# Kernel optimization log

Measured on AMD Instinct MI355X. Metric: run time of the kernel, lower is better.

Reference implementation:

```python
import jax, jax.numpy as jnp
import numpy as np

N_HEAD = 16
HEAD_DIM = 64  # n_embd // n_head = 1024 // 16


def setup_inputs() -> dict:
    key = jax.random.key(0)
    k1, k2, k3 = jax.random.split(key, 3)
    B, S, D = 2, 2048, 1024
    x = jax.random.normal(k1, (B, S, D), dtype=jnp.float32)
    # torch nn.Linear stores weight [out, in]; we keep [in, out] for x @ W
    w_qkv = jax.random.normal(k2, (D, 3 * D), dtype=jnp.float32) * (D ** -0.5)
    w_proj = jax.random.normal(k3, (D, D), dtype=jnp.float32) * (D ** -0.5)
    return {"x": x, "w_qkv": w_qkv, "w_proj": w_proj}


def reference(x, w_qkv, w_proj):
    B, S, D = x.shape
    qkv = x @ w_qkv  # [B, S, 3D]
    q, k, v = jnp.split(qkv, 3, axis=-1)
    # [B, H, S, hd]
    q = q.reshape(B, S, N_HEAD, HEAD_DIM).transpose(0, 2, 1, 3)
    k = k.reshape(B, S, N_HEAD, HEAD_DIM).transpose(0, 2, 1, 3)
    v = v.reshape(B, S, N_HEAD, HEAD_DIM).transpose(0, 2, 1, 3)
    att = jnp.einsum('bhid,bhjd->bhij', q, k) * (HEAD_DIM ** -0.5)
    causal = jnp.tril(jnp.ones((S, S), dtype=bool))
    att = jnp.where(causal, att, jnp.finfo(att.dtype).min)
    att = jax.nn.softmax(att, axis=-1)
    # dropout p=0 (eval) -> identity
    y = jnp.einsum('bhij,bhjd->bhid', att, v)
    y = y.transpose(0, 2, 1, 3).reshape(B, S, D)
    return y @ w_proj
```

## Files before the change

kernel.cpp:

```cpp
#include <hip/hip_runtime.h>

#define AS1 __attribute__((address_space(1)))
#define AS3 __attribute__((address_space(3)))

using f32x4 = __attribute__((ext_vector_type(4))) float;
using s16x8 = __attribute__((ext_vector_type(8))) short;
using u16x4 = __attribute__((ext_vector_type(4))) unsigned short;
using u32x2 = __attribute__((ext_vector_type(2))) unsigned int;

__device__ __forceinline__ unsigned short f2bf(float f) {
  union { float f; unsigned u; } v; v.f = f;
  unsigned u = v.u;
  return (unsigned short)((u + 0x7FFFu + ((u >> 16) & 1u)) >> 16);
}

__device__ __forceinline__ unsigned pack_bf2(float a, float b) {
  union { float f; unsigned u; } x, y; x.f = a; y.f = b;
  return (x.u >> 16) | (y.u & 0xFFFF0000u);
}

__device__ __forceinline__ void load_lds16(const void* g, void* l) {
  __builtin_amdgcn_global_load_lds((const AS1 void*)g, (AS3 void*)l, 16, 0, 0);
}

__global__ __launch_bounds__(256) void prep_kernel(const float* __restrict__ x,
                                                   const float* __restrict__ w_qkv,
                                                   const float* __restrict__ w_proj,
                                                   unsigned short* __restrict__ xb,
                                                   unsigned short* __restrict__ wqkvT,
                                                   unsigned short* __restrict__ wprojT) {
  __shared__ float tile[32][33];
  const int bid = blockIdx.x, tid = threadIdx.x;
  if (bid < 4096) {
    int i = bid * 256 + tid;
    float4 v = ((const float4*)x)[i];
    u16x4 o;
    o.x = f2bf(v.x); o.y = f2bf(v.y); o.z = f2bf(v.z); o.w = f2bf(v.w);
    ((u16x4*)xb)[i] = o;
    return;
  }
  const float* in;
  unsigned short* out;
  int bx, by, R, C;
  if (bid < 7168) {
    int t = bid - 4096;
    bx = t % 96; by = t / 96; R = 1024; C = 3072;
    in = w_qkv; out = wqkvT;
  } else {
    int t = bid - 7168;
    bx = t % 32; by = t / 32; R = 1024; C = 1024;
    in = w_proj; out = wprojT;
  }
  const int tx = tid & 31, ty = tid >> 5;
  int xcol = bx * 32 + tx;
  int y0 = by * 32;
  for (int j = ty; j < 32; j += 8)
    tile[j][tx] = in[(size_t)(y0 + j) * C + xcol];
  __syncthreads();
  int x2 = by * 32 + tx;
  int y2 = bx * 32;
  for (int j = ty; j < 32; j += 8)
    out[(size_t)(y2 + j) * R + x2] = f2bf(tile[tx][j]);
}

__global__ __launch_bounds__(256) void transpose_v(const unsigned short* __restrict__ qkv,
                                                   unsigned short* __restrict__ Vt) {
  __shared__ unsigned short tile[64][65];
  const int tid = threadIdx.x;
  const int bh = blockIdx.y, b = bh >> 4, h = bh & 15;
  const int s0 = blockIdx.x * 64;
#pragma unroll
  for (int it = 0; it < 2; ++it) {
    int c = tid + it * 256;
    int row = c >> 3, cc = c & 7;
    s16x8 v = *(const s16x8*)(qkv + (size_t)(b * 2048 + s0 + row) * 3072 + 2048 + h * 64 + cc * 8);
#pragma unroll
    for (int j = 0; j < 8; ++j) tile[row][cc * 8 + j] = (unsigned short)v[j];
  }
  __syncthreads();
#pragma unroll
  for (int it = 0; it < 2; ++it) {
    int c = tid + it * 256;
    int d = c >> 3, sc = c & 7;
    s16x8 o;
#pragma unroll
    for (int j = 0; j < 8; ++j) o[j] = (short)tile[sc * 8 + j][d];
    *(s16x8*)(Vt + (size_t)bh * 64 * 2048 + (size_t)d * 2048 + s0 + sc * 8) = o;
  }
}

__global__ __launch_bounds__(256) void gemm_qkv(const unsigned short* __restrict__ A,
                                                const unsigned short* __restrict__ Bt,
                                                unsigned short* __restrict__ C,
                                                int M, int N, int K) {
  __shared__ unsigned short As[128 * 64];
  __shared__ unsigned short Bs[128 * 64];
  const int tid = threadIdx.x;
  const int wave = tid >> 6, lane = tid & 63;
  const int l15 = lane & 15, quad = lane >> 4;
  const int sx = l15 & 7;
  const int wm = wave & 1, wn = wave >> 1;
  const int bm = blockIdx.y, bn = blockIdx.x;

  f32x4 acc[4][4] = {};

  for (int k0 = 0; k0 < K; k0 += 64) {
    __syncthreads();
#pragma unroll
    for (int s = 0; s < 4; ++s) {
      int c = tid + s * 256;
      int row = c >> 3, cc = c & 7;
      int kc = (cc ^ (row & 7)) * 8;
      load_lds16(A + (size_t)(bm * 128 + row) * K + k0 + kc, As + c * 8);
      load_lds16(Bt + (size_t)(bn * 128 + row) * K + k0 + kc, Bs + c * 8);
    }
    __syncthreads();
#pragma unroll
    for (int kk = 0; kk < 2; ++kk) {
      s16x8 af[4], bfr[4];
#pragma unroll
      for (int i = 0; i < 4; ++i) {
        af[i]  = *(const s16x8*)(As + (wm * 64 + i * 16 + l15) * 64 + ((quad + 4 * kk) ^ sx) * 8);
        bfr[i] = *(const s16x8*)(Bs + (wn * 64 + i * 16 + l15) * 64 + ((quad + 4 * kk) ^ sx) * 8);
      }
#pragma unroll
      for (int i = 0; i < 4; ++i)
#pragma unroll
        for (int j = 0; j < 4; ++j)
          acc[i][j] = __builtin_amdgcn_mfma_f32_16x16x32_bf16(af[i], bfr[j], acc[i][j], 0, 0, 0);
    }
  }

  const int row0 = bm * 128 + wm * 64 + quad * 4;
  const int col0 = bn * 128 + wn * 64 + l15;
#pragma unroll
  for (int i = 0; i < 4; ++i)
#pragma unroll
    for (int j = 0; j < 4; ++j)
#pragma unroll
      for (int r = 0; r < 4; ++r)
        C[(size_t)(row0 + i * 16 + r) * N + (col0 + j * 16)] = f2bf(acc[i][j][r]);
}

__global__ __launch_bounds__(256) void gemm_proj(const unsigned short* __restrict__ A,
                                                 const unsigned short* __restrict__ Bt,
                                                 float* __restrict__ C,
                                                 int M, int N, int K) {
  __shared__ unsigned short As[128 * 64];
  __shared__ unsigned short Bs[64 * 64];
  const int tid = threadIdx.x;
  const int wave = tid >> 6, lane = tid & 63;
  const int l15 = lane & 15, quad = lane >> 4;
  const int sx = l15 & 7;
  const int wm = wave & 1, wn = wave >> 1;
  const int bm = blockIdx.y, bn = blockIdx.x;

  f32x4 acc[4][2] = {};

  for (int k0 = 0; k0 < K; k0 += 64) {
    __syncthreads();
#pragma unroll
    for (int s = 0; s < 4; ++s) {
      int c = tid + s * 256;
      int row = c >> 3, cc = c & 7;
      int kc = (cc ^ (row & 7)) * 8;
      load_lds16(A + (size_t)(bm * 128 + row) * K + k0 + kc, As + c * 8);
    }
#pragma unroll
    for (int s = 0; s < 2; ++s) {
      int c = tid + s * 256;
      int row = c >> 3, cc = c & 7;
      int kc = (cc ^ (row & 7)) * 8;
      load_lds16(Bt + (size_t)(bn * 64 + row) * K + k0 + kc, Bs + c * 8);
    }
    __syncthreads();
#pragma unroll
    for (int kk = 0; kk < 2; ++kk) {
      s16x8 af[4], bfr[2];
#pragma unroll
      for (int i = 0; i < 4; ++i)
        af[i] = *(const s16x8*)(As + (wm * 64 + i * 16 + l15) * 64 + ((quad + 4 * kk) ^ sx) * 8);
#pragma unroll
      for (int j = 0; j < 2; ++j)
        bfr[j] = *(const s16x8*)(Bs + (wn * 32 + j * 16 + l15) * 64 + ((quad + 4 * kk) ^ sx) * 8);
#pragma unroll
      for (int i = 0; i < 4; ++i)
#pragma unroll
        for (int j = 0; j < 2; ++j)
          acc[i][j] = __builtin_amdgcn_mfma_f32_16x16x32_bf16(af[i], bfr[j], acc[i][j], 0, 0, 0);
    }
  }

  const int row0 = bm * 128 + wm * 64 + quad * 4;
  const int col0 = bn * 64 + wn * 32 + l15;
#pragma unroll
  for (int i = 0; i < 4; ++i)
#pragma unroll
    for (int j = 0; j < 2; ++j)
#pragma unroll
      for (int r = 0; r < 4; ++r)
        C[(size_t)(row0 + i * 16 + r) * N + (col0 + j * 16)] = acc[i][j][r];
}

__global__ __launch_bounds__(512) void attn_kernel(const unsigned short* __restrict__ qkv,
                                                   const unsigned short* __restrict__ Vt,
                                                   unsigned short* __restrict__ Y) {
  __shared__ unsigned short Qs[128 * 64];
  __shared__ unsigned short Ks[2][64 * 64];
  __shared__ unsigned short Vs[2][64 * 64];
  const int tid = threadIdx.x;
  const int wave = tid >> 6, lane = tid & 63;
  const int l15 = lane & 15, quad = lane >> 4;
  const int sx = l15 & 7, sx2 = sx << 1;

  const int p = blockIdx.x;
  const int r_ = p >> 8, c_ = p & 255;
  const int m_ = c_ & 15, g_ = c_ >> 4;
  const int bh = g_ + 16 * r_;
  const int lq = r_ ? (15 - m_) : m_;
  const int q0 = lq * 128;
  const int b = bh >> 4, h = bh & 15;
  const size_t base = (size_t)b * 2048 * 3072 + h * 64;
  const size_t vbase = (size_t)bh * 64 * 2048;

  const int srow = tid >> 3, scc = tid & 7;
  const int skc = (scc ^ (srow & 7)) * 8;

#pragma unroll
  for (int s = 0; s < 2; ++s) {
    int cid = tid + s * 512;
    int row = cid >> 3, cc = cid & 7;
    int kc = (cc ^ (row & 7)) * 8;
    load_lds16(qkv + base + (size_t)(q0 + row) * 3072 + kc, Qs + cid * 8);
  }
  load_lds16(qkv + base + (size_t)srow * 3072 + 1024 + skc, Ks[0] + tid * 8);
  load_lds16(Vt + vbase + (size_t)srow * 2048 + skc, Vs[0] + tid * 8);
  __syncthreads();

  s16x8 qf[2];
  qf[0] = *(const s16x8*)(Qs + (wave * 16 + l15) * 64 + ((quad    ) ^ sx) * 8);
  qf[1] = *(const s16x8*)(Qs + (wave * 16 + l15) * 64 + ((quad + 4) ^ sx) * 8);

  f32x4 o[4] = {};
  float m_i = -1e30f, l_i = 0.f;
  const float kScale = 0.125f * 1.44269504f;
  const int qrow_w0 = q0 + wave * 16;
  const int qrow = qrow_w0 + l15;
  unsigned short* Pw = Qs + wave * 16 * 64;

  const int jmax = q0 + 64;
  int cur = 0;

  for (int j0 = 0; j0 <= jmax; j0 += 64) {
    if (j0 < jmax) {
      load_lds16(qkv + base + (size_t)(j0 + 64 + srow) * 3072 + 1024 + skc, Ks[cur ^ 1] + tid * 8);
      load_lds16(Vt + vbase + (size_t)srow * 2048 + (j0 + 64) + skc, Vs[cur ^ 1] + tid * 8);
    }

    if (j0 <= qrow_w0 + 15) {
      const unsigned short* Kc = Ks[cur];
      const unsigned short* Vc = Vs[cur];
      f32x4 s[4];
#pragma unroll
      for (int nt = 0; nt < 4; ++nt) {
        const int kr = nt * 16 + l15;
        s16x8 kf0 = *(const s16x8*)(Kc + kr * 64 + ((quad    ) ^ sx) * 8);
        s16x8 kf1 = *(const s16x8*)(Kc + kr * 64 + ((quad + 4) ^ sx) * 8);
        f32x4 z = {};
        z = __builtin_amdgcn_mfma_f32_16x16x32_bf16(kf0, qf[0], z, 0, 0, 0);
        z = __builtin_amdgcn_mfma_f32_16x16x32_bf16(kf1, qf[1], z, 0, 0, 0);
        s[nt] = z;
      }

      if (j0 + 63 > qrow_w0) {
#pragma unroll
        for (int nt = 0; nt < 4; ++nt) {
          int key0 = j0 + nt * 16 + quad * 4;
#pragma unroll
          for (int r = 0; r < 4; ++r)
            if (key0 + r > qrow) s[nt][r] = -3e38f;
        }
      }

      float t0 = fmaxf(fmaxf(s[0][0], s[0][1]), fmaxf(s[0][2], s[0][3]));
      float t1 = fmaxf(fmaxf(s[1][0], s[1][1]), fmaxf(s[1][2], s[1][3]));
      float t2 = fmaxf(fmaxf(s[2][0], s[2][1]), fmaxf(s[2][2], s[2][3]));
      float t3 = fmaxf(fmaxf(s[3][0], s[3][1]), fmaxf(s[3][2], s[3][3]));
      float tmax = fmaxf(fmaxf(t0, t1), fmaxf(t2, t3));
      tmax = fmaxf(tmax, __shfl_xor(tmax, 16, 64));
      tmax = fmaxf(tmax, __shfl_xor(tmax, 32, 64));
      float mn = fmaxf(m_i, tmax);
      float alpha = __builtin_amdgcn_exp2f((m_i - mn) * kScale);
      m_i = mn;
      const float mk = mn * kScale;
      float rs[4] = {0.f, 0.f, 0.f, 0.f};
#pragma unroll
      for (int nt = 0; nt < 4; ++nt)
#pragma unroll
        for (int r = 0; r < 4; ++r) {
          float pv = __builtin_amdgcn_exp2f(__builtin_fmaf(s[nt][r], kScale, -mk));
          s[nt][r] = pv;
          rs[nt] += pv;
        }
      float rsum = (rs[0] + rs[1]) + (rs[2] + rs[3]);
      rsum += __shfl_xor(rsum, 16, 64);
      rsum += __shfl_xor(rsum, 32, 64);
      l_i = l_i * alpha + rsum;
#pragma unroll
      for (int dt = 0; dt < 4; ++dt)
#pragma unroll
        for (int r = 0; r < 4; ++r)
          o[dt][r] *= alpha;

#pragma unroll
      for (int nt = 0; nt < 4; ++nt) {
        u32x2 pk;
        pk.x = pack_bf2(s[nt][0], s[nt][1]);
        pk.y = pack_bf2(s[nt][2], s[nt][3]);
        int phys = (nt * 4 + quad) ^ sx2;
        *(u32x2*)(Pw + l15 * 64 + phys * 4) = pk;
      }

      s16x8 pf[2];
      pf[0] = *(const s16x8*)(Pw + l15 * 64 + (((quad * 2)    ) ^ sx2) * 4);
      pf[1] = *(const s16x8*)(Pw + l15 * 64 + (((quad * 2) + 8) ^ sx2) * 4);

#pragma unroll
      for (int dt = 0; dt < 4; ++dt) {
        const int vr = dt * 16 + l15;
        s16x8 vf0 = *(const s16x8*)(Vc + vr * 64 + ((quad    ) ^ sx) * 8);
        s16x8 vf1 = *(const s16x8*)(Vc + vr * 64 + ((quad + 4) ^ sx) * 8);
        o[dt] = __builtin_amdgcn_mfma_f32_16x16x32_bf16(vf0, pf[0], o[dt], 0, 0, 0);
        o[dt] = __builtin_amdgcn_mfma_f32_16x16x32_bf16(vf1, pf[1], o[dt], 0, 0, 0);
      }
    }

    __syncthreads();
    cur ^= 1;
  }

  const float inv = 1.0f / l_i;
  const size_t yoff = (size_t)(b * 2048 + qrow) * 1024 + h * 64 + quad * 4;
#pragma unroll
  for (int dt = 0; dt < 4; ++dt) {
    u16x4 pk;
#pragma unroll
    for (int r = 0; r < 4; ++r) pk[r] = f2bf(o[dt][r] * inv);
    *(u16x4*)(Y + yoff + dt * 16) = pk;
  }
}

extern "C" void kernel_launch(void* const* d_in, const int* in_sizes, int n_in,
                              void* d_out, int out_size, void* d_ws, size_t ws_size,
                              hipStream_t stream) {
  const float* x      = (const float*)d_in[0];
  const float* w_qkv  = (const float*)d_in[1];
  const float* w_proj = (const float*)d_in[2];
  char* ws = (char*)d_ws;
  unsigned short* xb     = (unsigned short*)(ws);
  unsigned short* wqkvT  = (unsigned short*)(ws + (size_t)(8  << 20));
  unsigned short* wprojT = (unsigned short*)(ws + (size_t)(14 << 20));
  unsigned short* qkv    = (unsigned short*)(ws + (size_t)(16 << 20));
  unsigned short* y      = (unsigned short*)(ws + (size_t)(40 << 20));
  unsigned short* Vt     = (unsigned short*)(ws + (size_t)(48 << 20));

  prep_kernel<<<8192, 256, 0, stream>>>(x, w_qkv, w_proj, xb, wqkvT, wprojT);
  gemm_qkv<<<dim3(24, 32), 256, 0, stream>>>(xb, wqkvT, qkv, 4096, 3072, 1024);
  transpose_v<<<dim3(32, 32), 256, 0, stream>>>(qkv, Vt);
  attn_kernel<<<512, 512, 0, stream>>>(qkv, Vt, y);
  gemm_proj<<<dim3(16, 32), 256, 0, stream>>>(y, wprojT, (float*)d_out, 4096, 1024, 1024);
}
```

Before: 178.4 us.

## Halve attention query tile to 64 rows and skip redundant softmax rescales

The attention kernel now processes 64 query rows per block with 4 waves instead of 128 rows with 8 waves, and launches twice as many blocks with a new causal load-balancing order. This drops the per-wave causal skip branch, since all waves in a block now share the same key range. The online-softmax rescale of the output and running sum is skipped when no row's max increases, which removes exp and multiply work on most iterations. In exchange each K/V tile is loaded by twice as many blocks, and the per-block pipeline is shorter.

```diff
diff --git a/kernel.cpp b/kernel.cpp
--- a/kernel.cpp
+++ b/kernel.cpp
@@ -202,10 +202,10 @@
         C[(size_t)(row0 + i * 16 + r) * N + (col0 + j * 16)] = acc[i][j][r];
 }
 
-__global__ __launch_bounds__(512) void attn_kernel(const unsigned short* __restrict__ qkv,
+__global__ __launch_bounds__(256) void attn_kernel(const unsigned short* __restrict__ qkv,
                                                    const unsigned short* __restrict__ Vt,
                                                    unsigned short* __restrict__ Y) {
-  __shared__ unsigned short Qs[128 * 64];
+  __shared__ unsigned short Qs[64 * 64];
   __shared__ unsigned short Ks[2][64 * 64];
   __shared__ unsigned short Vs[2][64 * 64];
   const int tid = threadIdx.x;
@@ -214,27 +214,24 @@
   const int sx = l15 & 7, sx2 = sx << 1;
 
   const int p = blockIdx.x;
-  const int r_ = p >> 8, c_ = p & 255;
-  const int m_ = c_ & 15, g_ = c_ >> 4;
-  const int bh = g_ + 16 * r_;
-  const int lq = r_ ? (15 - m_) : m_;
-  const int q0 = lq * 128;
+  const int bh = p & 31;
+  const int u = (p >> 5) & 7;
+  const int hi = p >> 8;
+  const int lq = (hi == 0) ? u : (hi == 1) ? (15 - u) : (hi == 2) ? (16 + u) : (31 - u);
+  const int q0 = lq * 64;
   const int b = bh >> 4, h = bh & 15;
   const size_t base = (size_t)b * 2048 * 3072 + h * 64;
   const size_t vbase = (size_t)bh * 64 * 2048;
 
-  const int srow = tid >> 3, scc = tid & 7;
-  const int skc = (scc ^ (srow & 7)) * 8;
-
 #pragma unroll
   for (int s = 0; s < 2; ++s) {
-    int cid = tid + s * 512;
-    int row = cid >> 3, cc = cid & 7;
+    int c = tid + s * 256;
+    int row = c >> 3, cc = c & 7;
     int kc = (cc ^ (row & 7)) * 8;
-    load_lds16(qkv + base + (size_t)(q0 + row) * 3072 + kc, Qs + cid * 8);
-  }
-  load_lds16(qkv + base + (size_t)srow * 3072 + 1024 + skc, Ks[0] + tid * 8);
-  load_lds16(Vt + vbase + (size_t)srow * 2048 + skc, Vs[0] + tid * 8);
+    load_lds16(qkv + base + (size_t)(q0 + row) * 3072 + kc, Qs + c * 8);
+    load_lds16(qkv + base + (size_t)row * 3072 + 1024 + kc, Ks[0] + c * 8);
+    load_lds16(Vt + vbase + (size_t)row * 2048 + kc, Vs[0] + c * 8);
+  }
   __syncthreads();
 
   s16x8 qf[2];
@@ -248,91 +245,97 @@
   const int qrow = qrow_w0 + l15;
   unsigned short* Pw = Qs + wave * 16 * 64;
 
-  const int jmax = q0 + 64;
   int cur = 0;
-
-  for (int j0 = 0; j0 <= jmax; j0 += 64) {
-    if (j0 < jmax) {
-      load_lds16(qkv + base + (size_t)(j0 + 64 + srow) * 3072 + 1024 + skc, Ks[cur ^ 1] + tid * 8);
-      load_lds16(Vt + vbase + (size_t)srow * 2048 + (j0 + 64) + skc, Vs[cur ^ 1] + tid * 8);
-    }
-
-    if (j0 <= qrow_w0 + 15) {
-      const unsigned short* Kc = Ks[cur];
-      const unsigned short* Vc = Vs[cur];
-      f32x4 s[4];
+  for (int j0 = 0; j0 <= q0; j0 += 64) {
+    if (j0 < q0) {
+#pragma unroll
+      for (int s = 0; s < 2; ++s) {
+        int c = tid + s * 256;
+        int row = c >> 3, cc = c & 7;
+        int kc = (cc ^ (row & 7)) * 8;
+        load_lds16(qkv + base + (size_t)(j0 + 64 + row) * 3072 + 1024 + kc, Ks[cur ^ 1] + c * 8);
+        load_lds16(Vt + vbase + (size_t)row * 2048 + (j0 + 64) + kc, Vs[cur ^ 1] + c * 8);
+      }
+    }
+
+    const unsigned short* Kc = Ks[cur];
+    const unsigned short* Vc = Vs[cur];
+    f32x4 s[4];
+#pragma unroll
+    for (int nt = 0; nt < 4; ++nt) {
+      const int kr = nt * 16 + l15;
+      s16x8 kf0 = *(const s16x8*)(Kc + kr * 64 + ((quad    ) ^ sx) * 8);
+      s16x8 kf1 = *(const s16x8*)(Kc + kr * 64 + ((quad + 4) ^ sx) * 8);
+      f32x4 z = {};
+      z = __builtin_amdgcn_mfma_f32_16x16x32_bf16(kf0, qf[0], z, 0, 0, 0);
+      z = __builtin_amdgcn_mfma_f32_16x16x32_bf16(kf1, qf[1], z, 0, 0, 0);
+      s[nt] = z;
+    }
+
+    if (j0 + 63 > qrow_w0) {
 #pragma unroll
       for (int nt = 0; nt < 4; ++nt) {
-        const int kr = nt * 16 + l15;
-        s16x8 kf0 = *(const s16x8*)(Kc + kr * 64 + ((quad    ) ^ sx) * 8);
-        s16x8 kf1 = *(const s16x8*)(Kc + kr * 64 + ((quad + 4) ^ sx) * 8);
-        f32x4 z = {};
-        z = __builtin_amdgcn_mfma_f32_16x16x32_bf16(kf0, qf[0], z, 0, 0, 0);
-        z = __builtin_amdgcn_mfma_f32_16x16x32_bf16(kf1, qf[1], z, 0, 0, 0);
-        s[nt] = z;
+        int key0 = j0 + nt * 16 + quad * 4;
+#pragma unroll
+        for (int r = 0; r < 4; ++r)
+          if (key0 + r > qrow) s[nt][r] = -3e38f;
       }
-
-      if (j0 + 63 > qrow_w0) {
-#pragma unroll
-        for (int nt = 0; nt < 4; ++nt) {
-          int key0 = j0 + nt * 16 + quad * 4;
-#pragma unroll
-          for (int r = 0; r < 4; ++r)
-            if (key0 + r > qrow) s[nt][r] = -3e38f;
-        }
-      }
-
-      float t0 = fmaxf(fmaxf(s[0][0], s[0][1]), fmaxf(s[0][2], s[0][3]));
-      float t1 = fmaxf(fmaxf(s[1][0], s[1][1]), fmaxf(s[1][2], s[1][3]));
-      float t2 = fmaxf(fmaxf(s[2][0], s[2][1]), fmaxf(s[2][2], s[2][3]));
-      float t3 = fmaxf(fmaxf(s[3][0], s[3][1]), fmaxf(s[3][2], s[3][3]));
-      float tmax = fmaxf(fmaxf(t0, t1), fmaxf(t2, t3));
-      tmax = fmaxf(tmax, __shfl_xor(tmax, 16, 64));
-      tmax = fmaxf(tmax, __shfl_xor(tmax, 32, 64));
+    }
+
+    float t0 = fmaxf(fmaxf(s[0][0], s[0][1]), fmaxf(s[0][2], s[0][3]));
+    float t1 = fmaxf(fmaxf(s[1][0], s[1][1]), fmaxf(s[1][2], s[1][3]));
+    float t2 = fmaxf(fmaxf(s[2][0], s[2][1]), fmaxf(s[2][2], s[2][3]));
+    float t3 = fmaxf(fmaxf(s[3][0], s[3][1]), fmaxf(s[3][2], s[3][3]));
+    float tmax = fmaxf(fmaxf(t0, t1), fmaxf(t2, t3));
+    tmax = fmaxf(tmax, __shfl_xor(tmax, 16, 64));
+    tmax = fmaxf(tmax, __shfl_xor(tmax, 32, 64));
+
+    if (!__all(tmax <= m_i)) {
       float mn = fmaxf(m_i, tmax);
       float alpha = __builtin_amdgcn_exp2f((m_i - mn) * kScale);
       m_i = mn;
-      const float mk = mn * kScale;
-      float rs[4] = {0.f, 0.f, 0.f, 0.f};
-#pragma unroll
-      for (int nt = 0; nt < 4; ++nt)
-#pragma unroll
-        for (int r = 0; r < 4; ++r) {
-          float pv = __builtin_amdgcn_exp2f(__builtin_fmaf(s[nt][r], kScale, -mk));
-          s[nt][r] = pv;
-          rs[nt] += pv;
-        }
-      float rsum = (rs[0] + rs[1]) + (rs[2] + rs[3]);
-      rsum += __shfl_xor(rsum, 16, 64);
-      rsum += __shfl_xor(rsum, 32, 64);
-      l_i = l_i * alpha + rsum;
+      l_i *= alpha;
 #pragma unroll
       for (int dt = 0; dt < 4; ++dt)
 #pragma unroll
         for (int r = 0; r < 4; ++r)
           o[dt][r] *= alpha;
-
-#pragma unroll
-      for (int nt = 0; nt < 4; ++nt) {
-        u32x2 pk;
-        pk.x = pack_bf2(s[nt][0], s[nt][1]);
-        pk.y = pack_bf2(s[nt][2], s[nt][3]);
-        int phys = (nt * 4 + quad) ^ sx2;
-        *(u32x2*)(Pw + l15 * 64 + phys * 4) = pk;
+    }
+    const float mk = m_i * kScale;
+    float rs[4] = {0.f, 0.f, 0.f, 0.f};
+#pragma unroll
+    for (int nt = 0; nt < 4; ++nt)
+#pragma unroll
+      for (int r = 0; r < 4; ++r) {
+        float pv = __builtin_amdgcn_exp2f(__builtin_fmaf(s[nt][r], kScale, -mk));
+        s[nt][r] = pv;
+        rs[nt] += pv;
       }
-
-      s16x8 pf[2];
-      pf[0] = *(const s16x8*)(Pw + l15 * 64 + (((quad * 2)    ) ^ sx2) * 4);
-      pf[1] = *(const s16x8*)(Pw + l15 * 64 + (((quad * 2) + 8) ^ sx2) * 4);
-
-#pragma unroll
-      for (int dt = 0; dt < 4; ++dt) {
-        const int vr = dt * 16 + l15;
-        s16x8 vf0 = *(const s16x8*)(Vc + vr * 64 + ((quad    ) ^ sx) * 8);
-        s16x8 vf1 = *(const s16x8*)(Vc + vr * 64 + ((quad + 4) ^ sx) * 8);
-        o[dt] = __builtin_amdgcn_mfma_f32_16x16x32_bf16(vf0, pf[0], o[dt], 0, 0, 0);
-        o[dt] = __builtin_amdgcn_mfma_f32_16x16x32_bf16(vf1, pf[1], o[dt], 0, 0, 0);
-      }
+    float rsum = (rs[0] + rs[1]) + (rs[2] + rs[3]);
+    rsum += __shfl_xor(rsum, 16, 64);
+    rsum += __shfl_xor(rsum, 32, 64);
+    l_i += rsum;
+
+#pragma unroll
+    for (int nt = 0; nt < 4; ++nt) {
+      u32x2 pk;
+      pk.x = pack_bf2(s[nt][0], s[nt][1]);
+      pk.y = pack_bf2(s[nt][2], s[nt][3]);
+      int phys = (nt * 4 + quad) ^ sx2;
+      *(u32x2*)(Pw + l15 * 64 + phys * 4) = pk;
+    }
+
+    s16x8 pf[2];
+    pf[0] = *(const s16x8*)(Pw + l15 * 64 + (((quad * 2)    ) ^ sx2) * 4);
+    pf[1] = *(const s16x8*)(Pw + l15 * 64 + (((quad * 2) + 8) ^ sx2) * 4);
+
+#pragma unroll
+    for (int dt = 0; dt < 4; ++dt) {
+      const int vr = dt * 16 + l15;
+      s16x8 vf0 = *(const s16x8*)(Vc + vr * 64 + ((quad    ) ^ sx) * 8);
+      s16x8 vf1 = *(const s16x8*)(Vc + vr * 64 + ((quad + 4) ^ sx) * 8);
+      o[dt] = __builtin_amdgcn_mfma_f32_16x16x32_bf16(vf0, pf[0], o[dt], 0, 0, 0);
+      o[dt] = __builtin_amdgcn_mfma_f32_16x16x32_bf16(vf1, pf[1], o[dt], 0, 0, 0);
     }
 
     __syncthreads();
@@ -367,6 +370,6 @@
   prep_kernel<<<8192, 256, 0, stream>>>(x, w_qkv, w_proj, xb, wqkvT, wprojT);
   gemm_qkv<<<dim3(24, 32), 256, 0, stream>>>(xb, wqkvT, qkv, 4096, 3072, 1024);
   transpose_v<<<dim3(32, 32), 256, 0, stream>>>(qkv, Vt);
-  attn_kernel<<<512, 512, 0, stream>>>(qkv, Vt, y);
+  attn_kernel<<<1024, 256, 0, stream>>>(qkv, Vt, y);
   gemm_proj<<<dim3(16, 32), 256, 0, stream>>>(y, wprojT, (float*)d_out, 4096, 1024, 1024);
 }
```

Result: slower. 191.1 us (+7.1%).

## Double-buffer LDS in both GEMMs and enlarge their output tiles

Applied to the files above, without the earlier changes.

Both projection GEMMs now prefetch the next K-slice into a second LDS buffer while MFMAs run on the current one. Synchronisation uses raw s_barrier plus an s_waitcnt vmcnt(8) in place of two __syncthreads per iteration. The QKV GEMM grows to a 256x256 tile with 512 threads. The output-projection GEMM grows from 128x64 to a 128x128 tile. This is meant to hide global-load latency and raise arithmetic intensity, but it leaves only 192 QKV blocks and 256 proj blocks, which risks idle CUs on a 256-CU device. It also raises LDS use to 128KB per QKV block.

```diff
diff --git a/kernel.cpp b/kernel.cpp
--- a/kernel.cpp
+++ b/kernel.cpp
@@ -89,12 +89,12 @@
   }
 }
 
-__global__ __launch_bounds__(256) void gemm_qkv(const unsigned short* __restrict__ A,
+__global__ __launch_bounds__(512) void gemm_qkv(const unsigned short* __restrict__ A,
                                                 const unsigned short* __restrict__ Bt,
                                                 unsigned short* __restrict__ C,
                                                 int M, int N, int K) {
-  __shared__ unsigned short As[128 * 64];
-  __shared__ unsigned short Bs[128 * 64];
+  __shared__ unsigned short As[2][256 * 64];
+  __shared__ unsigned short Bs[2][256 * 64];
   const int tid = threadIdx.x;
   const int wave = tid >> 6, lane = tid & 63;
   const int l15 = lane & 15, quad = lane >> 4;
@@ -102,39 +102,62 @@
   const int wm = wave & 1, wn = wave >> 1;
   const int bm = blockIdx.y, bn = blockIdx.x;
 
-  f32x4 acc[4][4] = {};
-
-  for (int k0 = 0; k0 < K; k0 += 64) {
-    __syncthreads();
-#pragma unroll
-    for (int s = 0; s < 4; ++s) {
-      int c = tid + s * 256;
-      int row = c >> 3, cc = c & 7;
-      int kc = (cc ^ (row & 7)) * 8;
-      load_lds16(A + (size_t)(bm * 128 + row) * K + k0 + kc, As + c * 8);
-      load_lds16(Bt + (size_t)(bn * 128 + row) * K + k0 + kc, Bs + c * 8);
-    }
-    __syncthreads();
+  f32x4 acc[8][4] = {};
+  const int T = K >> 6;
+
+#pragma unroll
+  for (int s = 0; s < 4; ++s) {
+    int c = tid + s * 512;
+    int row = c >> 3, cc = c & 7;
+    int kc = (cc ^ (row & 7)) * 8;
+    load_lds16(A + (size_t)(bm * 256 + row) * K + kc, As[0] + c * 8);
+    load_lds16(Bt + (size_t)(bn * 256 + row) * K + kc, Bs[0] + c * 8);
+  }
+
+  for (int t = 0; t < T; ++t) {
+    const int cur = t & 1;
+    __builtin_amdgcn_s_barrier();
+    __builtin_amdgcn_sched_barrier(0);
+    if (t + 1 < T) {
+      const int k1 = (t + 1) << 6;
+#pragma unroll
+      for (int s = 0; s < 4; ++s) {
+        int c = tid + s * 512;
+        int row = c >> 3, cc = c & 7;
+        int kc = (cc ^ (row & 7)) * 8;
+        load_lds16(A + (size_t)(bm * 256 + row) * K + k1 + kc, As[cur ^ 1] + c * 8);
+        load_lds16(Bt + (size_t)(bn * 256 + row) * K + k1 + kc, Bs[cur ^ 1] + c * 8);
+      }
+      asm volatile("s_waitcnt vmcnt(8)" ::: "memory");
+    } else {
+      asm volatile("s_waitcnt vmcnt(0)" ::: "memory");
+    }
+    __builtin_amdgcn_s_barrier();
+    __builtin_amdgcn_sched_barrier(0);
+
+    const unsigned short* Ab = As[cur];
+    const unsigned short* Bb = Bs[cur];
 #pragma unroll
     for (int kk = 0; kk < 2; ++kk) {
-      s16x8 af[4], bfr[4];
-#pragma unroll
-      for (int i = 0; i < 4; ++i) {
-        af[i]  = *(const s16x8*)(As + (wm * 64 + i * 16 + l15) * 64 + ((quad + 4 * kk) ^ sx) * 8);
-        bfr[i] = *(const s16x8*)(Bs + (wn * 64 + i * 16 + l15) * 64 + ((quad + 4 * kk) ^ sx) * 8);
-      }
-#pragma unroll
-      for (int i = 0; i < 4; ++i)
+      s16x8 af[8], bfr[4];
+#pragma unroll
+      for (int i = 0; i < 8; ++i)
+        af[i] = *(const s16x8*)(Ab + (wm * 128 + i * 16 + l15) * 64 + ((quad + 4 * kk) ^ sx) * 8);
+#pragma unroll
+      for (int j = 0; j < 4; ++j)
+        bfr[j] = *(const s16x8*)(Bb + (wn * 64 + j * 16 + l15) * 64 + ((quad + 4 * kk) ^ sx) * 8);
+#pragma unroll
+      for (int i = 0; i < 8; ++i)
 #pragma unroll
         for (int j = 0; j < 4; ++j)
           acc[i][j] = __builtin_amdgcn_mfma_f32_16x16x32_bf16(af[i], bfr[j], acc[i][j], 0, 0, 0);
     }
   }
 
-  const int row0 = bm * 128 + wm * 64 + quad * 4;
-  const int col0 = bn * 128 + wn * 64 + l15;
-#pragma unroll
-  for (int i = 0; i < 4; ++i)
+  const int row0 = bm * 256 + wm * 128 + quad * 4;
+  const int col0 = bn * 256 + wn * 64 + l15;
+#pragma unroll
+  for (int i = 0; i < 8; ++i)
 #pragma unroll
     for (int j = 0; j < 4; ++j)
 #pragma unroll
@@ -146,8 +169,8 @@
                                                  const unsigned short* __restrict__ Bt,
                                                  float* __restrict__ C,
                                                  int M, int N, int K) {
-  __shared__ unsigned short As[128 * 64];
-  __shared__ unsigned short Bs[64 * 64];
+  __shared__ unsigned short As[2][128 * 64];
+  __shared__ unsigned short Bs[2][128 * 64];
   const int tid = threadIdx.x;
   const int wave = tid >> 6, lane = tid & 63;
   const int l15 = lane & 15, quad = lane >> 4;
@@ -155,48 +178,64 @@
   const int wm = wave & 1, wn = wave >> 1;
   const int bm = blockIdx.y, bn = blockIdx.x;
 
-  f32x4 acc[4][2] = {};
-
-  for (int k0 = 0; k0 < K; k0 += 64) {
-    __syncthreads();
-#pragma unroll
-    for (int s = 0; s < 4; ++s) {
-      int c = tid + s * 256;
-      int row = c >> 3, cc = c & 7;
-      int kc = (cc ^ (row & 7)) * 8;
-      load_lds16(A + (size_t)(bm * 128 + row) * K + k0 + kc, As + c * 8);
-    }
-#pragma unroll
-    for (int s = 0; s < 2; ++s) {
-      int c = tid + s * 256;
-      int row = c >> 3, cc = c & 7;
-      int kc = (cc ^ (row & 7)) * 8;
-      load_lds16(Bt + (size_t)(bn * 64 + row) * K + k0 + kc, Bs + c * 8);
-    }
-    __syncthreads();
+  f32x4 acc[4][4] = {};
+  const int T = K >> 6;
+
+#pragma unroll
+  for (int s = 0; s < 4; ++s) {
+    int c = tid + s * 256;
+    int row = c >> 3, cc = c & 7;
+    int kc = (cc ^ (row & 7)) * 8;
+    load_lds16(A + (size_t)(bm * 128 + row) * K + kc, As[0] + c * 8);
+    load_lds16(Bt + (size_t)(bn * 128 + row) * K + kc, Bs[0] + c * 8);
+  }
+
+  for (int t = 0; t < T; ++t) {
+    const int cur = t & 1;
+    __builtin_amdgcn_s_barrier();
+    __builtin_amdgcn_sched_barrier(0);
+    if (t + 1 < T) {
+      const int k1 = (t + 1) << 6;
+#pragma unroll
+      for (int s = 0; s < 4; ++s) {
+        int c = tid + s * 256;
+        int row = c >> 3, cc = c & 7;
+        int kc = (cc ^ (row & 7)) * 8;
+        load_lds16(A + (size_t)(bm * 128 + row) * K + k1 + kc, As[cur ^ 1] + c * 8);
+        load_lds16(Bt + (size_t)(bn * 128 + row) * K + k1 + kc, Bs[cur ^ 1] + c * 8);
+      }
+      asm volatile("s_waitcnt vmcnt(8)" ::: "memory");
+    } else {
+      asm volatile("s_waitcnt vmcnt(0)" ::: "memory");
+    }
+    __builtin_amdgcn_s_barrier();
+    __builtin_amdgcn_sched_barrier(0);
+
+    const unsigned short* Ab = As[cur];
+    const unsigned short* Bb = Bs[cur];
 #pragma unroll
     for (int kk = 0; kk < 2; ++kk) {
-      s16x8 af[4], bfr[2];
+      s16x8 af[4], bfr[4];
 #pragma unroll
       for (int i = 0; i < 4; ++i)
-        af[i] = *(const s16x8*)(As + (wm * 64 + i * 16 + l15) * 64 + ((quad + 4 * kk) ^ sx) * 8);
-#pragma unroll
-      for (int j = 0; j < 2; ++j)
-        bfr[j] = *(const s16x8*)(Bs + (wn * 32 + j * 16 + l15) * 64 + ((quad + 4 * kk) ^ sx) * 8);
+        af[i] = *(const s16x8*)(Ab + (wm * 64 + i * 16 + l15) * 64 + ((quad + 4 * kk) ^ sx) * 8);
+#pragma unroll
+      for (int j = 0; j < 4; ++j)
+        bfr[j] = *(const s16x8*)(Bb + (wn * 64 + j * 16 + l15) * 64 + ((quad + 4 * kk) ^ sx) * 8);
 #pragma unroll
       for (int i = 0; i < 4; ++i)
 #pragma unroll
-        for (int j = 0; j < 2; ++j)
+        for (int j = 0; j < 4; ++j)
           acc[i][j] = __builtin_amdgcn_mfma_f32_16x16x32_bf16(af[i], bfr[j], acc[i][j], 0, 0, 0);
     }
   }
 
   const int row0 = bm * 128 + wm * 64 + quad * 4;
-  const int col0 = bn * 64 + wn * 32 + l15;
+  const int col0 = bn * 128 + wn * 64 + l15;
 #pragma unroll
   for (int i = 0; i < 4; ++i)
 #pragma unroll
-    for (int j = 0; j < 2; ++j)
+    for (int j = 0; j < 4; ++j)
 #pragma unroll
       for (int r = 0; r < 4; ++r)
         C[(size_t)(row0 + i * 16 + r) * N + (col0 + j * 16)] = acc[i][j][r];
@@ -292,7 +331,7 @@
       float mn = fmaxf(m_i, tmax);
       float alpha = __builtin_amdgcn_exp2f((m_i - mn) * kScale);
       m_i = mn;
-      const float mk = mn * kScale;
+      const float mk = m_i * kScale;
       float rs[4] = {0.f, 0.f, 0.f, 0.f};
 #pragma unroll
       for (int nt = 0; nt < 4; ++nt)
@@ -365,8 +404,8 @@
   unsigned short* Vt     = (unsigned short*)(ws + (size_t)(48 << 20));
 
   prep_kernel<<<8192, 256, 0, stream>>>(x, w_qkv, w_proj, xb, wqkvT, wprojT);
-  gemm_qkv<<<dim3(24, 32), 256, 0, stream>>>(xb, wqkvT, qkv, 4096, 3072, 1024);
+  gemm_qkv<<<dim3(12, 16), 512, 0, stream>>>(xb, wqkvT, qkv, 4096, 3072, 1024);
   transpose_v<<<dim3(32, 32), 256, 0, stream>>>(qkv, Vt);
   attn_kernel<<<512, 512, 0, stream>>>(qkv, Vt, y);
-  gemm_proj<<<dim3(16, 32), 256, 0, stream>>>(y, wprojT, (float*)d_out, 4096, 1024, 1024);
-}
+  gemm_proj<<<dim3(8, 32), 256, 0, stream>>>(y, wprojT, (float*)d_out, 4096, 1024, 1024);
+}
```

Measured after the change: 188.4 us. 1.06x slower.

## Widen attention KV tile to 128 keys and add occupancy launch bound

Applied to the files above, without the earlier changes.

The attention loop now processes 128 keys per iteration instead of 64. K and V double buffers grow to 128-key tiles, V uses a 128-wide swizzled layout, and P is staged to LDS in two 64-key halves. The goal is to halve the number of loop iterations, barriers and online-softmax rescales per query block. In exchange it uses more LDS and registers (eight score fragments per wave). It also drops the per-wave skip of fully masked tiles, so some waves do masked work on the diagonal tile. A launch_bounds minimum-blocks hint of 4 is added to steer register allocation toward higher occupancy.

```diff
diff --git a/kernel.cpp b/kernel.cpp
--- a/kernel.cpp
+++ b/kernel.cpp
@@ -202,12 +202,12 @@
         C[(size_t)(row0 + i * 16 + r) * N + (col0 + j * 16)] = acc[i][j][r];
 }
 
-__global__ __launch_bounds__(512) void attn_kernel(const unsigned short* __restrict__ qkv,
-                                                   const unsigned short* __restrict__ Vt,
-                                                   unsigned short* __restrict__ Y) {
+__global__ __launch_bounds__(512, 4) void attn_kernel(const unsigned short* __restrict__ qkv,
+                                                      const unsigned short* __restrict__ Vt,
+                                                      unsigned short* __restrict__ Y) {
   __shared__ unsigned short Qs[128 * 64];
-  __shared__ unsigned short Ks[2][64 * 64];
-  __shared__ unsigned short Vs[2][64 * 64];
+  __shared__ unsigned short Ks[2][128 * 64];
+  __shared__ unsigned short Vs[2][64 * 128];
   const int tid = threadIdx.x;
   const int wave = tid >> 6, lane = tid & 63;
   const int l15 = lane & 15, quad = lane >> 4;
@@ -223,18 +223,18 @@
   const size_t base = (size_t)b * 2048 * 3072 + h * 64;
   const size_t vbase = (size_t)bh * 64 * 2048;
 
-  const int srow = tid >> 3, scc = tid & 7;
-  const int skc = (scc ^ (srow & 7)) * 8;
-
-#pragma unroll
-  for (int s = 0; s < 2; ++s) {
-    int cid = tid + s * 512;
-    int row = cid >> 3, cc = cid & 7;
-    int kc = (cc ^ (row & 7)) * 8;
-    load_lds16(qkv + base + (size_t)(q0 + row) * 3072 + kc, Qs + cid * 8);
-  }
-  load_lds16(qkv + base + (size_t)srow * 3072 + 1024 + skc, Ks[0] + tid * 8);
-  load_lds16(Vt + vbase + (size_t)srow * 2048 + skc, Vs[0] + tid * 8);
+  const int c0 = tid, c1 = tid + 512;
+  const int kr0 = c0 >> 3, kc0 = ((c0 & 7) ^ (kr0 & 7)) * 8;
+  const int kr1 = c1 >> 3, kc1 = ((c1 & 7) ^ (kr1 & 7)) * 8;
+  const int vr0 = c0 >> 4, vc0 = ((c0 & 15) ^ (vr0 & 7)) * 8;
+  const int vr1 = c1 >> 4, vc1 = ((c1 & 15) ^ (vr1 & 7)) * 8;
+
+  load_lds16(qkv + base + (size_t)(q0 + kr0) * 3072 + kc0, Qs + c0 * 8);
+  load_lds16(qkv + base + (size_t)(q0 + kr1) * 3072 + kc1, Qs + c1 * 8);
+  load_lds16(qkv + base + (size_t)kr0 * 3072 + 1024 + kc0, Ks[0] + c0 * 8);
+  load_lds16(qkv + base + (size_t)kr1 * 3072 + 1024 + kc1, Ks[0] + c1 * 8);
+  load_lds16(Vt + vbase + (size_t)vr0 * 2048 + vc0, Vs[0] + c0 * 8);
+  load_lds16(Vt + vbase + (size_t)vr1 * 2048 + vc1, Vs[0] + c1 * 8);
   __syncthreads();
 
   s16x8 qf[2];
@@ -248,90 +248,95 @@
   const int qrow = qrow_w0 + l15;
   unsigned short* Pw = Qs + wave * 16 * 64;
 
-  const int jmax = q0 + 64;
   int cur = 0;
-
-  for (int j0 = 0; j0 <= jmax; j0 += 64) {
-    if (j0 < jmax) {
-      load_lds16(qkv + base + (size_t)(j0 + 64 + srow) * 3072 + 1024 + skc, Ks[cur ^ 1] + tid * 8);
-      load_lds16(Vt + vbase + (size_t)srow * 2048 + (j0 + 64) + skc, Vs[cur ^ 1] + tid * 8);
-    }
-
-    if (j0 <= qrow_w0 + 15) {
-      const unsigned short* Kc = Ks[cur];
-      const unsigned short* Vc = Vs[cur];
-      f32x4 s[4];
-#pragma unroll
-      for (int nt = 0; nt < 4; ++nt) {
-        const int kr = nt * 16 + l15;
-        s16x8 kf0 = *(const s16x8*)(Kc + kr * 64 + ((quad    ) ^ sx) * 8);
-        s16x8 kf1 = *(const s16x8*)(Kc + kr * 64 + ((quad + 4) ^ sx) * 8);
-        f32x4 z = {};
-        z = __builtin_amdgcn_mfma_f32_16x16x32_bf16(kf0, qf[0], z, 0, 0, 0);
-        z = __builtin_amdgcn_mfma_f32_16x16x32_bf16(kf1, qf[1], z, 0, 0, 0);
-        s[nt] = z;
+  for (int t = 0; t <= lq; ++t) {
+    const int j0 = t << 7;
+    if (t < lq) {
+      const int j1 = j0 + 128;
+      load_lds16(qkv + base + (size_t)(j1 + kr0) * 3072 + 1024 + kc0, Ks[cur ^ 1] + c0 * 8);
+      load_lds16(qkv + base + (size_t)(j1 + kr1) * 3072 + 1024 + kc1, Ks[cur ^ 1] + c1 * 8);
+      load_lds16(Vt + vbase + (size_t)vr0 * 2048 + j1 + vc0, Vs[cur ^ 1] + c0 * 8);
+      load_lds16(Vt + vbase + (size_t)vr1 * 2048 + j1 + vc1, Vs[cur ^ 1] + c1 * 8);
+    }
+
+    const unsigned short* Kc = Ks[cur];
+    const unsigned short* Vc = Vs[cur];
+
+    f32x4 s[8];
+#pragma unroll
+    for (int nt = 0; nt < 8; ++nt) {
+      const int kr = nt * 16 + l15;
+      s16x8 kf0 = *(const s16x8*)(Kc + kr * 64 + ((quad    ) ^ sx) * 8);
+      s16x8 kf1 = *(const s16x8*)(Kc + kr * 64 + ((quad + 4) ^ sx) * 8);
+      f32x4 z = {};
+      z = __builtin_amdgcn_mfma_f32_16x16x32_bf16(kf0, qf[0], z, 0, 0, 0);
+      z = __builtin_amdgcn_mfma_f32_16x16x32_bf16(kf1, qf[1], z, 0, 0, 0);
+      s[nt] = z;
+    }
+
+    if (j0 + 127 > qrow_w0) {
+#pragma unroll
+      for (int nt = 0; nt < 8; ++nt) {
+        int key0 = j0 + nt * 16 + quad * 4;
+#pragma unroll
+        for (int r = 0; r < 4; ++r)
+          if (key0 + r > qrow) s[nt][r] = -3e38f;
       }
-
-      if (j0 + 63 > qrow_w0) {
-#pragma unroll
-        for (int nt = 0; nt < 4; ++nt) {
-          int key0 = j0 + nt * 16 + quad * 4;
-#pragma unroll
-          for (int r = 0; r < 4; ++r)
-            if (key0 + r > qrow) s[nt][r] = -3e38f;
-        }
-      }
-
-      float t0 = fmaxf(fmaxf(s[0][0], s[0][1]), fmaxf(s[0][2], s[0][3]));
-      float t1 = fmaxf(fmaxf(s[1][0], s[1][1]), fmaxf(s[1][2], s[1][3]));
-      float t2 = fmaxf(fmaxf(s[2][0], s[2][1]), fmaxf(s[2][2], s[2][3]));
-      float t3 = fmaxf(fmaxf(s[3][0], s[3][1]), fmaxf(s[3][2], s[3][3]));
-      float tmax = fmaxf(fmaxf(t0, t1), fmaxf(t2, t3));
-      tmax = fmaxf(tmax, __shfl_xor(tmax, 16, 64));
-      tmax = fmaxf(tmax, __shfl_xor(tmax, 32, 64));
-      float mn = fmaxf(m_i, tmax);
-      float alpha = __builtin_amdgcn_exp2f((m_i - mn) * kScale);
-      m_i = mn;
-      const float mk = mn * kScale;
-      float rs[4] = {0.f, 0.f, 0.f, 0.f};
-#pragma unroll
-      for (int nt = 0; nt < 4; ++nt)
-#pragma unroll
-        for (int r = 0; r < 4; ++r) {
-          float pv = __builtin_amdgcn_exp2f(__builtin_fmaf(s[nt][r], kScale, -mk));
-          s[nt][r] = pv;
-          rs[nt] += pv;
-        }
-      float rsum = (rs[0] + rs[1]) + (rs[2] + rs[3]);
-      rsum += __shfl_xor(rsum, 16, 64);
-      rsum += __shfl_xor(rsum, 32, 64);
-      l_i = l_i * alpha + rsum;
-#pragma unroll
-      for (int dt = 0; dt < 4; ++dt)
-#pragma unroll
-        for (int r = 0; r < 4; ++r)
-          o[dt][r] *= alpha;
-
-#pragma unroll
-      for (int nt = 0; nt < 4; ++nt) {
+    }
+
+    float gm[8];
+#pragma unroll
+    for (int nt = 0; nt < 8; ++nt)
+      gm[nt] = fmaxf(fmaxf(s[nt][0], s[nt][1]), fmaxf(s[nt][2], s[nt][3]));
+    float tmax = fmaxf(fmaxf(fmaxf(gm[0], gm[1]), fmaxf(gm[2], gm[3])),
+                       fmaxf(fmaxf(gm[4], gm[5]), fmaxf(gm[6], gm[7])));
+    tmax = fmaxf(tmax, __shfl_xor(tmax, 16, 64));
+    tmax = fmaxf(tmax, __shfl_xor(tmax, 32, 64));
+    float mn = fmaxf(m_i, tmax);
+    float alpha = __builtin_amdgcn_exp2f((m_i - mn) * kScale);
+    m_i = mn;
+    const float mk = mn * kScale;
+    float rs[8];
+#pragma unroll
+    for (int nt = 0; nt < 8; ++nt) {
+      float a0 = __builtin_amdgcn_exp2f(__builtin_fmaf(s[nt][0], kScale, -mk));
+      float a1 = __builtin_amdgcn_exp2f(__builtin_fmaf(s[nt][1], kScale, -mk));
+      float a2 = __builtin_amdgcn_exp2f(__builtin_fmaf(s[nt][2], kScale, -mk));
+      float a3 = __builtin_amdgcn_exp2f(__builtin_fmaf(s[nt][3], kScale, -mk));
+      s[nt][0] = a0; s[nt][1] = a1; s[nt][2] = a2; s[nt][3] = a3;
+      rs[nt] = (a0 + a1) + (a2 + a3);
+    }
+    float rsum = ((rs[0] + rs[1]) + (rs[2] + rs[3])) + ((rs[4] + rs[5]) + (rs[6] + rs[7]));
+    rsum += __shfl_xor(rsum, 16, 64);
+    rsum += __shfl_xor(rsum, 32, 64);
+    l_i = l_i * alpha + rsum;
+#pragma unroll
+    for (int dt = 0; dt < 4; ++dt)
+#pragma unroll
+      for (int r = 0; r < 4; ++r)
+        o[dt][r] *= alpha;
+
+#pragma unroll
+    for (int hh = 0; hh < 2; ++hh) {
+#pragma unroll
+      for (int n2 = 0; n2 < 4; ++n2) {
+        const int nt = hh * 4 + n2;
         u32x2 pk;
         pk.x = pack_bf2(s[nt][0], s[nt][1]);
         pk.y = pack_bf2(s[nt][2], s[nt][3]);
-        int phys = (nt * 4 + quad) ^ sx2;
+        const int phys = (n2 * 4 + quad) ^ sx2;
         *(u32x2*)(Pw + l15 * 64 + phys * 4) = pk;
       }
-
-      s16x8 pf[2];
-      pf[0] = *(const s16x8*)(Pw + l15 * 64 + (((quad * 2)    ) ^ sx2) * 4);
-      pf[1] = *(const s16x8*)(Pw + l15 * 64 + (((quad * 2) + 8) ^ sx2) * 4);
-
+      s16x8 pf0 = *(const s16x8*)(Pw + l15 * 64 + (((quad * 2)    ) ^ sx2) * 4);
+      s16x8 pf1 = *(const s16x8*)(Pw + l15 * 64 + (((quad * 2) + 8) ^ sx2) * 4);
 #pragma unroll
       for (int dt = 0; dt < 4; ++dt) {
-        const int vr = dt * 16 + l15;
-        s16x8 vf0 = *(const s16x8*)(Vc + vr * 64 + ((quad    ) ^ sx) * 8);
-        s16x8 vf1 = *(const s16x8*)(Vc + vr * 64 + ((quad + 4) ^ sx) * 8);
-        o[dt] = __builtin_amdgcn_mfma_f32_16x16x32_bf16(vf0, pf[0], o[dt], 0, 0, 0);
-        o[dt] = __builtin_amdgcn_mfma_f32_16x16x32_bf16(vf1, pf[1], o[dt], 0, 0, 0);
+        const int d = dt * 16 + l15;
+        const int dx = d & 7;
+        s16x8 vf0 = *(const s16x8*)(Vc + d * 128 + (hh * 8 + ((quad    ) ^ dx)) * 8);
+        s16x8 vf1 = *(const s16x8*)(Vc + d * 128 + (hh * 8 + ((quad + 4) ^ dx)) * 8);
+        o[dt] = __builtin_amdgcn_mfma_f32_16x16x32_bf16(vf0, pf0, o[dt], 0, 0, 0);
+        o[dt] = __builtin_amdgcn_mfma_f32_16x16x32_bf16(vf1, pf1, o[dt], 0, 0, 0);
       }
     }
 
```

After: 174.0 us. -2.5%, faster.
